# Kernel tuning notes

Measured on AMD Instinct MI355X. Metric: run time of the kernel, lower is better.

## Reference

```python
import jax, jax.numpy as jnp
import numpy as np

N_NODES = 65536
N_EDGES = 262144
N_GRAPHS = 2048
NF = 16   # num_node_features
EF = 6    # num_edge_features
H1, H2, H3 = 32, 16, 8  # conv1 out, conv2 out, lin1 out


def _lin_init(key, fan_in, fan_out):
    kw, kb = jax.random.split(key)
    s = 1.0 / np.sqrt(fan_in)
    w = jax.random.uniform(kw, (fan_in, fan_out), minval=-s, maxval=s, dtype=jnp.float32)
    b = jax.random.uniform(kb, (fan_out,), minval=-s, maxval=s, dtype=jnp.float32)
    return w, b


def setup_inputs() -> dict:
    key = jax.random.key(0)
    ks = jax.random.split(key, 16)
    inp = {}
    inp["x_p"] = jax.random.normal(ks[0], (N_NODES, NF), dtype=jnp.float32)
    inp["x_d"] = jax.random.normal(ks[1], (4, NF), dtype=jnp.float32)  # unused by forward
    inp["edge_attr_p"] = jax.random.uniform(ks[2], (N_EDGES, EF), dtype=jnp.float32)
    inp["edge_attr_d"] = jax.random.uniform(ks[3], (4, EF), dtype=jnp.float32)  # unused
    inp["edge_index_p"] = jax.random.randint(ks[4], (2, N_EDGES), 0, N_NODES, dtype=jnp.int32)
    inp["x_p_batch"] = jnp.sort(jax.random.randint(ks[5], (N_NODES,), 0, N_GRAPHS, dtype=jnp.int32))
    # conv1: NNConv(NF, 32); edge nn: Linear(EF,16) -> ReLU -> Linear(16, NF*32)
    inp["nn1_w1"], inp["nn1_b1"] = _lin_init(ks[6], EF, 16)
    inp["nn1_w2"], inp["nn1_b2"] = _lin_init(ks[7], 16, NF * H1)
    inp["root1"] = _lin_init(ks[8], NF, H1)[0]
    inp["bias1"] = jnp.zeros((H1,), dtype=jnp.float32)
    # conv2: NNConv(32, 16); edge nn: Linear(EF,16) -> ReLU -> Linear(16, 32*16)
    inp["nn2_w1"], inp["nn2_b1"] = _lin_init(ks[9], EF, 16)
    inp["nn2_w2"], inp["nn2_b2"] = _lin_init(ks[10], 16, H1 * H2)
    inp["root2"] = _lin_init(ks[11], H1, H2)[0]
    inp["bias2"] = jnp.zeros((H2,), dtype=jnp.float32)
    # attention pooling gate: Linear(NF,NF) -> ReLU -> Linear(NF,1)
    inp["gate_w1"], inp["gate_b1"] = _lin_init(ks[12], NF, NF)
    inp["gate_w2"], inp["gate_b2"] = _lin_init(ks[13], NF, 1)
    # head: Linear(16+16, 8) -> Linear(8, 1)  (attention=True)
    inp["lin1_w"], inp["lin1_b"] = _lin_init(ks[14], H2 + NF, H3)
    inp["lin2_w"], inp["lin2_b"] = _lin_init(ks[15], H3, 1)
    return inp


def _nnconv(x, edge_attr, src, dst, w1, b1, w2, b2, root, bias, in_c, out_c, n_nodes):
    # per-edge dynamic weight matrix Theta(e) : [E, in_c, out_c]
    h = jax.nn.relu(edge_attr @ w1 + b1) @ w2 + b2
    w_dyn = h.reshape(-1, in_c, out_c)
    msg = jnp.einsum('ei,eio->eo', x[src], w_dyn)          # [E, out_c]
    agg = jax.ops.segment_sum(msg, dst, num_segments=n_nodes)  # scatter-add
    return agg + x @ root + bias


def _attention_pool(x, batch, gw1, gb1, gw2, gb2, n_graphs):
    g = (jax.nn.relu(x @ gw1 + gb1) @ gw2 + gb2)[:, 0]     # [N] gate logits
    m = jax.ops.segment_max(g, batch, num_segments=n_graphs)
    e = jnp.exp(g - m[batch])
    s = jax.ops.segment_sum(e, batch, num_segments=n_graphs)
    alpha = e / s[batch]                                    # per-graph softmax
    return jax.ops.segment_sum(alpha[:, None] * x, batch, num_segments=n_graphs)


def _mean_pool(x, batch, n_graphs):
    s = jax.ops.segment_sum(x, batch, num_segments=n_graphs)
    cnt = jax.ops.segment_sum(jnp.ones((x.shape[0],), x.dtype), batch, num_segments=n_graphs)
    return s / jnp.maximum(cnt, 1.0)[:, None]


def reference(x_p, x_d, edge_attr_p, edge_attr_d, edge_index_p, x_p_batch,
              nn1_w1, nn1_b1, nn1_w2, nn1_b2, root1, bias1,
              nn2_w1, nn2_b1, nn2_w2, nn2_b2, root2, bias2,
              gate_w1, gate_b1, gate_w2, gate_b2,
              lin1_w, lin1_b, lin2_w, lin2_b):
    src, dst = edge_index_p[0], edge_index_p[1]
    # attention pooling on raw node features (attention=True)
    x_att = _attention_pool(x_p, x_p_batch, gate_w1, gate_b1, gate_w2, gate_b2, N_GRAPHS)
    # two NNConv layers with ReLU
    h = jax.nn.relu(_nnconv(x_p, edge_attr_p, src, dst, nn1_w1, nn1_b1, nn1_w2, nn1_b2,
                            root1, bias1, NF, H1, N_NODES))
    h = jax.nn.relu(_nnconv(h, edge_attr_p, src, dst, nn2_w1, nn2_b1, nn2_w2, nn2_b2,
                            root2, bias2, H1, H2, N_NODES))
    g = _mean_pool(h, x_p_batch, N_GRAPHS)                  # [B, 16]
    g = jnp.concatenate([g, x_att], axis=1)                 # [B, 32]
    # dropout p=0.5 is identity in eval mode
    g = g @ lin1_w + lin1_b
    out = g @ lin2_w + lin2_b                               # [B, 1]
    return out
```

## Files before the change

kernel.cpp:

```cpp
#include <hip/hip_runtime.h>

#define NN 65536
#define NE 262144
#define NG 2048

typedef __attribute__((ext_vector_type(16))) float f32x16;
typedef __attribute__((ext_vector_type(4)))  float f32x4;
typedef __attribute__((ext_vector_type(8)))  __bf16 bf16x8;

__device__ inline unsigned pack2(float a, float b) {
    return __builtin_amdgcn_perm(__float_as_uint(b), __float_as_uint(a), 0x07060302u);
}
__device__ inline float lof(float p) {
    return p - __uint_as_float(__float_as_uint(p) & 0xffff0000u);
}
__device__ inline bf16x8 asb(uint4 u) { return __builtin_bit_cast(bf16x8, u); }

__global__ __launch_bounds__(256) void k_setup(
    const int* __restrict__ batch,
    const float* __restrict__ w2a, const float* __restrict__ b2a,
    const float* __restrict__ w2b, const float* __restrict__ b2c,
    int* __restrict__ cnt, int* __restrict__ cur, int* __restrict__ goffs,
    unsigned* __restrict__ f1, unsigned* __restrict__ f2)
{
    int t = blockIdx.x * 256 + threadIdx.x;
    if (t < NN) { cnt[t] = 0; cur[t] = 0; }
    if (t <= NG) {
        int lo = 0, hi = NN;
        while (lo < hi) {
            int mid = (lo + hi) >> 1;
            if (batch[mid] < t) lo = mid + 1; else hi = mid;
        }
        goffs[t] = lo;
    }
    if (t < 17408) {
        int c = t / 8704;
        int r = t - c * 8704;
        int d = r & 3;
        int l = (r >> 2) & 63;
        int tt = (r >> 8) & 1;
        int s = r >> 9;
        if (c == 0) {
            int n = l & 31, g = l >> 5;
            int j0 = 2*d;
            int c0 = (g*8 + j0)*32 + n;
            int c1 = c0 + 32;
            float a = (s < 16) ? w2a[s*512 + c0] : b2a[c0];
            float b = (s < 16) ? w2a[s*512 + c1] : b2a[c1];
            f1[r] = tt ? pack2(lof(a), lof(b)) : pack2(a, b);
        } else {
            int n = l & 15, g = l >> 4;
            int j0 = 2*d;
            int c0 = (g*8 + j0)*16 + n;
            int c1 = c0 + 16;
            float a = (s < 16) ? w2b[s*512 + c0] : b2c[c0];
            float b = (s < 16) ? w2b[s*512 + c1] : b2c[c1];
            f2[r] = tt ? pack2(lof(a), lof(b)) : pack2(a, b);
        }
    }
}

__global__ __launch_bounds__(64) void k_gateatt(const float* __restrict__ x,
    const float* __restrict__ gw1, const float* __restrict__ gb1,
    const float* __restrict__ gw2, const float* __restrict__ gb2,
    const int* __restrict__ goffs, float* __restrict__ x_att)
{
    __shared__ float sw[256];
    __shared__ float sb[16];
    __shared__ float sw2[16];
    __shared__ float sb2;
    __shared__ float gb[1024];
    const int g = blockIdx.x;
    const int lane = threadIdx.x;
    for (int i = lane; i < 256; i += 64) sw[i] = gw1[i];
    if (lane < 16) { sb[lane] = gb1[lane]; sw2[lane] = gw2[lane]; }
    if (lane == 0) sb2 = gb2[0];
    const int s = goffs[g], e = goffs[g + 1];
    const int cnt = e - s;
    if (cnt <= 0) {
        if (lane < 16) x_att[g*16 + lane] = 0.f;
        return;
    }
    const int cap = cnt < 1024 ? cnt : 1024;
    __syncthreads();
    for (int ii = lane; ii < cap; ii += 64) {
        const float4* xp = (const float4*)(x + (size_t)(s + ii) * 16);
        float xv[16];
#pragma unroll
        for (int i = 0; i < 4; ++i) {
            float4 tt = xp[i];
            xv[4*i] = tt.x; xv[4*i+1] = tt.y; xv[4*i+2] = tt.z; xv[4*i+3] = tt.w;
        }
        float gv = sb2;
#pragma unroll
        for (int j = 0; j < 16; ++j) {
            float a = sb[j];
#pragma unroll
            for (int i = 0; i < 16; ++i) a += xv[i] * sw[i*16 + j];
            gv += fmaxf(a, 0.f) * sw2[j];
        }
        gb[ii] = gv;
    }
    __syncthreads();
    float m = -1e30f;
    for (int ii = lane; ii < cap; ii += 64) m = fmaxf(m, gb[ii]);
#pragma unroll
    for (int d = 32; d; d >>= 1) m = fmaxf(m, __shfl_xor(m, d));
    float sum = 0.f;
    for (int ii = lane; ii < cap; ii += 64) {
        float ev = expf(gb[ii] - m);
        gb[ii] = ev;
        sum += ev;
    }
#pragma unroll
    for (int d = 32; d; d >>= 1) sum += __shfl_xor(sum, d);
    const float inv = 1.f / sum;
    __syncthreads();
    const int f = lane & 15, sub = lane >> 4;
    float acc = 0.f;
    for (int ii = sub; ii < cap; ii += 4)
        acc += gb[ii] * inv * x[(size_t)(s + ii)*16 + f];
    acc += __shfl_xor(acc, 16);
    acc += __shfl_xor(acc, 32);
    if (lane < 16) x_att[g*16 + f] = acc;
}

__global__ __launch_bounds__(256) void k_hist(const int* __restrict__ ei, int* __restrict__ cnt)
{
    int e = blockIdx.x * 256 + threadIdx.x;
    if (e >= NE) return;
    atomicAdd(&cnt[ei[NE + e]], 1);
}

__global__ __launch_bounds__(256) void k_scan_blk(const int* __restrict__ cnt,
    int* __restrict__ offs, int* __restrict__ bsum)
{
    __shared__ int s[256];
    int t = threadIdx.x, b = blockIdx.x;
    int v = cnt[b*256 + t];
    s[t] = v;
    __syncthreads();
#pragma unroll
    for (int d = 1; d < 256; d <<= 1) {
        int add = (t >= d) ? s[t - d] : 0;
        __syncthreads();
        s[t] += add;
        __syncthreads();
    }
    offs[b*256 + t] = s[t] - v;
    if (t == 255) bsum[b] = s[255];
}

__global__ __launch_bounds__(256) void k_scan_top(const int* __restrict__ bsum,
    int* __restrict__ boff)
{
    __shared__ int s[256];
    int t = threadIdx.x;
    int v = bsum[t];
    s[t] = v;
    __syncthreads();
#pragma unroll
    for (int d = 1; d < 256; d <<= 1) {
        int add = (t >= d) ? s[t - d] : 0;
        __syncthreads();
        s[t] += add;
        __syncthreads();
    }
    boff[t] = s[t] - v;
}

__global__ __launch_bounds__(256) void k_scan_add(int* __restrict__ offs,
    const int* __restrict__ boff)
{
    int i = blockIdx.x * 256 + threadIdx.x;
    if (i == 0) offs[NN] = NE;
    if (i >= NN) return;
    offs[i] += boff[i >> 8];
}

__global__ __launch_bounds__(256) void k_scatter(const int* __restrict__ ei,
    const int* __restrict__ offs, int* __restrict__ cur,
    int* __restrict__ eperm, int* __restrict__ esrc)
{
    int e = blockIdx.x * 256 + threadIdx.x;
    if (e >= NE) return;
    int d = ei[NE + e];
    int pos = offs[d] + atomicAdd(&cur[d], 1);
    eperm[pos] = e;
    esrc[pos] = ei[e];
}

__global__ __launch_bounds__(256) void k_conv1(
    const float* __restrict__ x, const float* __restrict__ ea,
    const int* __restrict__ eperm, const int* __restrict__ esrc,
    const float* __restrict__ w1, const float* __restrict__ b1,
    const unsigned* __restrict__ bfrag, float* __restrict__ msg)
{
    const int tid  = threadIdx.x;
    const int lane = tid & 63;
    const int wid  = tid >> 6;
    const int m    = lane & 31;
    const int g    = lane >> 5;
    const uint4* bf4 = (const uint4*)bfrag;

    const int tile = blockIdx.x*4 + wid;
    const int p    = tile*32 + m;
    const int src  = esrc[p];
    const int e    = eperm[p];

    float xs[8];
    {
        const float4* xp = (const float4*)(x + (size_t)src*16 + g*8);
        float4 aa = xp[0], bb = xp[1];
        xs[0]=aa.x; xs[1]=aa.y; xs[2]=aa.z; xs[3]=aa.w;
        xs[4]=bb.x; xs[5]=bb.y; xs[6]=bb.z; xs[7]=bb.w;
    }
    float h[17];
    {
        const float2 e01 = *(const float2*)(ea + (size_t)e*6);
        const float2 e23 = *(const float2*)(ea + (size_t)e*6 + 2);
        const float2 e45 = *(const float2*)(ea + (size_t)e*6 + 4);
        const float a0=e01.x, a1=e01.y, a2=e23.x, a3=e23.y, a4=e45.x, a5=e45.y;
#pragma unroll
        for (int j = 0; j < 16; ++j) {
            float c = b1[j];
            c += a0*w1[0*16+j]; c += a1*w1[1*16+j]; c += a2*w1[2*16+j];
            c += a3*w1[3*16+j]; c += a4*w1[4*16+j]; c += a5*w1[5*16+j];
            h[j] = fmaxf(c, 0.f);
        }
        h[16] = 1.f;
    }

    f32x16 acc0 = {}, acc1 = {};
#pragma unroll
    for (int s = 0; s < 17; ++s) {
        const float hs = h[s];
        float p0 = hs*xs[0], p1 = hs*xs[1], p2 = hs*xs[2], p3 = hs*xs[3];
        float p4 = hs*xs[4], p5 = hs*xs[5], p6 = hs*xs[6], p7 = hs*xs[7];
        uint4 uh = { pack2(p0,p1), pack2(p2,p3), pack2(p4,p5), pack2(p6,p7) };
        uint4 ul = { pack2(lof(p0),lof(p1)), pack2(lof(p2),lof(p3)),
                     pack2(lof(p4),lof(p5)), pack2(lof(p6),lof(p7)) };
        uint4 wh = bf4[(s*2+0)*64 + lane];
        uint4 wl = bf4[(s*2+1)*64 + lane];
        if (s & 1) {
            acc1 = __builtin_amdgcn_mfma_f32_32x32x16_bf16(asb(uh), asb(wh), acc1, 0, 0, 0);
            acc1 = __builtin_amdgcn_mfma_f32_32x32x16_bf16(asb(uh), asb(wl), acc1, 0, 0, 0);
            acc1 = __builtin_amdgcn_mfma_f32_32x32x16_bf16(asb(ul), asb(wh), acc1, 0, 0, 0);
        } else {
            acc0 = __builtin_amdgcn_mfma_f32_32x32x16_bf16(asb(uh), asb(wh), acc0, 0, 0, 0);
            acc0 = __builtin_amdgcn_mfma_f32_32x32x16_bf16(asb(uh), asb(wl), acc0, 0, 0, 0);
            acc0 = __builtin_amdgcn_mfma_f32_32x32x16_bf16(asb(ul), asb(wh), acc0, 0, 0, 0);
        }
    }

    float* mbase = msg + (size_t)tile*32*32;
    const int rb = g*4;
#pragma unroll
    for (int r = 0; r < 16; ++r) {
        int mr = (r&3) + 8*(r>>2) + rb;
        mbase[(size_t)mr*32 + m] = acc0[r] + acc1[r];
    }
}

__global__ __launch_bounds__(256) void k_conv2(
    const float* __restrict__ x, const float* __restrict__ ea,
    const int* __restrict__ eperm, const int* __restrict__ esrc,
    const float* __restrict__ w1, const float* __restrict__ b1,
    const unsigned* __restrict__ bfrag, float* __restrict__ msg)
{
    __shared__ float lt[4][16*21];
    const int tid  = threadIdx.x;
    const int lane = tid & 63;
    const int wid  = tid >> 6;
    const int m    = lane & 15;
    const int g    = lane >> 4;
    const uint4* bf4 = (const uint4*)bfrag;

    const int tile = blockIdx.x*4 + wid;
    const int p    = tile*16 + m;
    const int src  = esrc[p];
    const int e    = eperm[p];

    uint4 xh, xl;
    {
        const float4* xp = (const float4*)(x + (size_t)src*32 + g*8);
        float4 aa = xp[0], bb = xp[1];
        float v0=aa.x, v1=aa.y, v2=aa.z, v3=aa.w, v4=bb.x, v5=bb.y, v6=bb.z, v7=bb.w;
        xh = (uint4){ pack2(v0,v1), pack2(v2,v3), pack2(v4,v5), pack2(v6,v7) };
        xl = (uint4){ pack2(lof(v0),lof(v1)), pack2(lof(v2),lof(v3)),
                      pack2(lof(v4),lof(v5)), pack2(lof(v6),lof(v7)) };
    }
    float h[17];
    {
        const float2 e01 = *(const float2*)(ea + (size_t)e*6);
        const float2 e23 = *(const float2*)(ea + (size_t)e*6 + 2);
        const float2 e45 = *(const float2*)(ea + (size_t)e*6 + 4);
        const float a0=e01.x, a1=e01.y, a2=e23.x, a3=e23.y, a4=e45.x, a5=e45.y;
#pragma unroll
        for (int j = 0; j < 16; ++j) {
            float c = b1[j];
            c += a0*w1[0*16+j]; c += a1*w1[1*16+j]; c += a2*w1[2*16+j];
            c += a3*w1[3*16+j]; c += a4*w1[4*16+j]; c += a5*w1[5*16+j];
            h[j] = fmaxf(c, 0.f);
        }
        h[16] = 1.f;
    }

    f32x4 macc = {};
#pragma unroll
    for (int s = 0; s < 17; ++s) {
        uint4 wh = bf4[(s*2+0)*64 + lane];
        uint4 wl = bf4[(s*2+1)*64 + lane];
        f32x4 t = {};
        t = __builtin_amdgcn_mfma_f32_16x16x32_bf16(asb(wh), asb(xh), t, 0, 0, 0);
        t = __builtin_amdgcn_mfma_f32_16x16x32_bf16(asb(wl), asb(xh), t, 0, 0, 0);
        t = __builtin_amdgcn_mfma_f32_16x16x32_bf16(asb(wh), asb(xl), t, 0, 0, 0);
        const float hs = h[s];
        macc.x += hs*t.x; macc.y += hs*t.y; macc.z += hs*t.z; macc.w += hs*t.w;
    }

    float* lw = lt[wid];
    lw[m*21 + g*4 + 0] = macc.x;
    lw[m*21 + g*4 + 1] = macc.y;
    lw[m*21 + g*4 + 2] = macc.z;
    lw[m*21 + g*4 + 3] = macc.w;
    asm volatile("s_waitcnt lgkmcnt(0)" ::: "memory");
    const int rrow = lane >> 2, fq = lane & 3;
    float o0 = lw[rrow*21 + fq*4 + 0];
    float o1 = lw[rrow*21 + fq*4 + 1];
    float o2 = lw[rrow*21 + fq*4 + 2];
    float o3 = lw[rrow*21 + fq*4 + 3];
    float4* mb = (float4*)(msg + (size_t)tile*256);
    mb[rrow*4 + fq] = make_float4(o0, o1, o2, o3);
}

__global__ __launch_bounds__(256) void k_reduce1(
    const float* __restrict__ msg, const int* __restrict__ offs,
    const float* __restrict__ x, const float* __restrict__ root,
    const float* __restrict__ bias, float* __restrict__ h1)
{
    __shared__ float s_r[512];
    __shared__ float s_b[32];
    int tid = threadIdx.x;
    for (int i = tid; i < 512; i += 256) s_r[i] = root[i];
    if (tid < 32) s_b[tid] = bias[tid];
    __syncthreads();
    int gid = blockIdx.x * 256 + tid;
    int n = gid >> 3, q = gid & 7;
    int s = offs[n], e = offs[n + 1];
    float4 acc = make_float4(s_b[4*q], s_b[4*q+1], s_b[4*q+2], s_b[4*q+3]);
    const float4* s_r4 = (const float4*)s_r;
    const float* xp = x + (size_t)n * 16;
#pragma unroll
    for (int i = 0; i < 16; ++i) {
        float xi = xp[i];
        float4 w = s_r4[i*8 + q];
        acc.x += xi*w.x; acc.y += xi*w.y; acc.z += xi*w.z; acc.w += xi*w.w;
    }
    for (int p = s; p < e; ++p) {
        float4 mr = ((const float4*)(msg + (size_t)p * 32))[q];
        acc.x += mr.x; acc.y += mr.y; acc.z += mr.z; acc.w += mr.w;
    }
    acc.x = fmaxf(acc.x, 0.f); acc.y = fmaxf(acc.y, 0.f);
    acc.z = fmaxf(acc.z, 0.f); acc.w = fmaxf(acc.w, 0.f);
    ((float4*)(h1 + (size_t)n * 32))[q] = acc;
}

__global__ __launch_bounds__(256) void k_reduce2(
    const float* __restrict__ msg, const int* __restrict__ offs,
    const float* __restrict__ h1, const float* __restrict__ root,
    const float* __restrict__ bias, float* __restrict__ h2)
{
    __shared__ float s_r[512];
    __shared__ float s_b[16];
    int tid = threadIdx.x;
    for (int i = tid; i < 512; i += 256) s_r[i] = root[i];
    if (tid < 16) s_b[tid] = bias[tid];
    __syncthreads();
    int gid = blockIdx.x * 256 + tid;
    int n = gid >> 2, q = gid & 3;
    int s = offs[n], e = offs[n + 1];
    float4 acc = make_float4(s_b[4*q], s_b[4*q+1], s_b[4*q+2], s_b[4*q+3]);
    const float4* s_r4 = (const float4*)s_r;
    const float* xp = h1 + (size_t)n * 32;
#pragma unroll
    for (int i = 0; i < 32; ++i) {
        float xi = xp[i];
        float4 w = s_r4[i*4 + q];
        acc.x += xi*w.x; acc.y += xi*w.y; acc.z += xi*w.z; acc.w += xi*w.w;
    }
    for (int p = s; p < e; ++p) {
        float4 mr = ((const float4*)(msg + (size_t)p * 16))[q];
        acc.x += mr.x; acc.y += mr.y; acc.z += mr.z; acc.w += mr.w;
    }
    acc.x = fmaxf(acc.x, 0.f); acc.y = fmaxf(acc.y, 0.f);
    acc.z = fmaxf(acc.z, 0.f); acc.w = fmaxf(acc.w, 0.f);
    ((float4*)(h2 + (size_t)n * 16))[q] = acc;
}

__global__ __launch_bounds__(64) void k_head(
    const float* __restrict__ h2, const float* __restrict__ x_att,
    const int* __restrict__ goffs,
    const float* __restrict__ l1w, const float* __restrict__ l1b,
    const float* __restrict__ l2w, const float* __restrict__ l2b,
    float* __restrict__ out)
{
    int g = blockIdx.x;
    int lane = threadIdx.x;
    int s = goffs[g], e = goffs[g + 1];
    __shared__ float v[32];
    __shared__ float hmid[8];
    int f = lane & 15, sub = lane >> 4;
    float acc = 0.f;
    for (int i = s + sub; i < e; i += 4) acc += h2[(size_t)i*16 + f];
    acc += __shfl_xor(acc, 16);
    acc += __shfl_xor(acc, 32);
    float cnt = fmaxf((float)(e - s), 1.0f);
    if (lane < 16) {
        v[lane]      = acc / cnt;
        v[16 + lane] = x_att[g*16 + lane];
    }
    __syncthreads();
    if (lane < 8) {
        float a = l1b[lane];
#pragma unroll
        for (int i = 0; i < 32; ++i) a += v[i] * l1w[i*8 + lane];
        hmid[lane] = a;
    }
    __syncthreads();
    if (lane == 0) {
        float a = l2b[0];
#pragma unroll
        for (int j = 0; j < 8; ++j) a += hmid[j] * l2w[j];
        out[g] = a;
    }
}

extern "C" void kernel_launch(void* const* d_in, const int* in_sizes, int n_in,
                              void* d_out, int out_size, void* d_ws, size_t ws_size,
                              hipStream_t stream) {
    const float* x_p    = (const float*)d_in[0];
    const float* ea_p   = (const float*)d_in[2];
    const int*   ei     = (const int*)d_in[4];
    const int*   batch  = (const int*)d_in[5];
    const float* nn1_w1 = (const float*)d_in[6];
    const float* nn1_b1 = (const float*)d_in[7];
    const float* nn1_w2 = (const float*)d_in[8];
    const float* nn1_b2 = (const float*)d_in[9];
    const float* root1  = (const float*)d_in[10];
    const float* bias1  = (const float*)d_in[11];
    const float* nn2_w1 = (const float*)d_in[12];
    const float* nn2_b1 = (const float*)d_in[13];
    const float* nn2_w2 = (const float*)d_in[14];
    const float* nn2_b2 = (const float*)d_in[15];
    const float* root2  = (const float*)d_in[16];
    const float* bias2  = (const float*)d_in[17];
    const float* gw1    = (const float*)d_in[18];
    const float* gb1    = (const float*)d_in[19];
    const float* gw2    = (const float*)d_in[20];
    const float* gb2    = (const float*)d_in[21];
    const float* l1w    = (const float*)d_in[22];
    const float* l1b    = (const float*)d_in[23];
    const float* l2w    = (const float*)d_in[24];
    const float* l2b    = (const float*)d_in[25];

    float*    h1     = (float*)d_ws;
    float*    h2     = h1 + (size_t)NN * 32;
    float*    x_att  = h2 + (size_t)NN * 16;
    int*      goffs  = (int*)(x_att + (size_t)NG * 16);
    int*      offs   = goffs + 2052;
    int*      cnt    = offs + 65540;
    int*      cur    = cnt + NN;
    int*      bsum   = cur + NN;
    int*      boff   = bsum + 256;
    int*      eperm  = boff + 256;
    int*      esrc   = eperm + NE;
    unsigned* bfrag1 = (unsigned*)(esrc + NE);
    unsigned* bfrag2 = bfrag1 + 8704;
    float*    msg    = (float*)(bfrag2 + 8704);

    k_setup<<<512, 256, 0, stream>>>(batch, nn1_w2, nn1_b2, nn2_w2, nn2_b2,
                                     cnt, cur, goffs, bfrag1, bfrag2);

    k_gateatt<<<NG, 64, 0, stream>>>(x_p, gw1, gb1, gw2, gb2, goffs, x_att);

    k_hist<<<NE/256, 256, 0, stream>>>(ei, cnt);
    k_scan_blk<<<NN/256, 256, 0, stream>>>(cnt, offs, bsum);
    k_scan_top<<<1, 256, 0, stream>>>(bsum, boff);
    k_scan_add<<<NN/256, 256, 0, stream>>>(offs, boff);
    k_scatter<<<NE/256, 256, 0, stream>>>(ei, offs, cur, eperm, esrc);

    k_conv1<<<2048, 256, 0, stream>>>(x_p, ea_p, eperm, esrc, nn1_w1, nn1_b1, bfrag1, msg);
    k_reduce1<<<NN*8/256, 256, 0, stream>>>(msg, offs, x_p, root1, bias1, h1);

    k_conv2<<<4096, 256, 0, stream>>>(h1, ea_p, eperm, esrc, nn2_w1, nn2_b1, bfrag2, msg);
    k_reduce2<<<NN*4/256, 256, 0, stream>>>(msg, offs, h1, root2, bias2, h2);

    k_head<<<NG, 64, 0, stream>>>(h2, x_att, goffs, l1w, l1b, l2w, l2b, (float*)d_out);
}
```

Measured before the change: 138.3 us.

## Factor edge weight out of conv1 MFMA, pack edge pairs, stage msg via LDS

In conv1 the per-edge hidden scalar is now applied after the matrix multiply. The MFMA computes W_s·x once per hidden slot and the result is scaled by h[s] in registers, so the per-step product, bf16 packing and hi/lo split are gone and x is converted only once. Edge permutation and source index are merged into one int2 array, so each conv kernel reads one coalesced word. Conv1 output is transposed through shared memory so messages are written with float4 stores, and both conv kernels get an occupancy hint in their launch bounds. This costs 16 extra vector FMAs per step and extra LDS traffic, and the change in operand roles and precision-split order could shift numerics slightly.

Result: slower. 391.7 us (+183.3%).

```diff
diff --git a/kernel.cpp b/kernel.cpp
--- a/kernel.cpp
+++ b/kernel.cpp
@@ -179,23 +179,22 @@
 }
 
 __global__ __launch_bounds__(256) void k_scatter(const int* __restrict__ ei,
-    const int* __restrict__ offs, int* __restrict__ cur,
-    int* __restrict__ eperm, int* __restrict__ esrc)
+    const int* __restrict__ offs, int* __restrict__ cur, int2* __restrict__ epair)
 {
     int e = blockIdx.x * 256 + threadIdx.x;
     if (e >= NE) return;
     int d = ei[NE + e];
     int pos = offs[d] + atomicAdd(&cur[d], 1);
-    eperm[pos] = e;
-    esrc[pos] = ei[e];
-}
-
-__global__ __launch_bounds__(256) void k_conv1(
+    epair[pos] = make_int2(e, ei[e]);
+}
+
+__global__ __launch_bounds__(256, 4) void k_conv1(
     const float* __restrict__ x, const float* __restrict__ ea,
-    const int* __restrict__ eperm, const int* __restrict__ esrc,
+    const int2* __restrict__ epair,
     const float* __restrict__ w1, const float* __restrict__ b1,
     const unsigned* __restrict__ bfrag, float* __restrict__ msg)
 {
+    __shared__ float lt[4][32*33];
     const int tid  = threadIdx.x;
     const int lane = tid & 63;
     const int wid  = tid >> 6;
@@ -205,15 +204,16 @@
 
     const int tile = blockIdx.x*4 + wid;
     const int p    = tile*32 + m;
-    const int src  = esrc[p];
-    const int e    = eperm[p];
-
-    float xs[8];
+    const int2 ep  = epair[p];
+    const int e    = ep.x, src = ep.y;
+
+    uint4 xh, xl;
     {
         const float4* xp = (const float4*)(x + (size_t)src*16 + g*8);
         float4 aa = xp[0], bb = xp[1];
-        xs[0]=aa.x; xs[1]=aa.y; xs[2]=aa.z; xs[3]=aa.w;
-        xs[4]=bb.x; xs[5]=bb.y; xs[6]=bb.z; xs[7]=bb.w;
+        xh = (uint4){ pack2(aa.x,aa.y), pack2(aa.z,aa.w), pack2(bb.x,bb.y), pack2(bb.z,bb.w) };
+        xl = (uint4){ pack2(lof(aa.x),lof(aa.y)), pack2(lof(aa.z),lof(aa.w)),
+                      pack2(lof(bb.x),lof(bb.y)), pack2(lof(bb.z),lof(bb.w)) };
     }
     float h[17];
     {
@@ -231,40 +231,40 @@
         h[16] = 1.f;
     }
 
-    f32x16 acc0 = {}, acc1 = {};
+    f32x16 acc = {};
 #pragma unroll
     for (int s = 0; s < 17; ++s) {
-        const float hs = h[s];
-        float p0 = hs*xs[0], p1 = hs*xs[1], p2 = hs*xs[2], p3 = hs*xs[3];
-        float p4 = hs*xs[4], p5 = hs*xs[5], p6 = hs*xs[6], p7 = hs*xs[7];
-        uint4 uh = { pack2(p0,p1), pack2(p2,p3), pack2(p4,p5), pack2(p6,p7) };
-        uint4 ul = { pack2(lof(p0),lof(p1)), pack2(lof(p2),lof(p3)),
-                     pack2(lof(p4),lof(p5)), pack2(lof(p6),lof(p7)) };
         uint4 wh = bf4[(s*2+0)*64 + lane];
         uint4 wl = bf4[(s*2+1)*64 + lane];
-        if (s & 1) {
-            acc1 = __builtin_amdgcn_mfma_f32_32x32x16_bf16(asb(uh), asb(wh), acc1, 0, 0, 0);
-            acc1 = __builtin_amdgcn_mfma_f32_32x32x16_bf16(asb(uh), asb(wl), acc1, 0, 0, 0);
-            acc1 = __builtin_amdgcn_mfma_f32_32x32x16_bf16(asb(ul), asb(wh), acc1, 0, 0, 0);
-        } else {
-            acc0 = __builtin_amdgcn_mfma_f32_32x32x16_bf16(asb(uh), asb(wh), acc0, 0, 0, 0);
-            acc0 = __builtin_amdgcn_mfma_f32_32x32x16_bf16(asb(uh), asb(wl), acc0, 0, 0, 0);
-            acc0 = __builtin_amdgcn_mfma_f32_32x32x16_bf16(asb(ul), asb(wh), acc0, 0, 0, 0);
-        }
-    }
-
-    float* mbase = msg + (size_t)tile*32*32;
-    const int rb = g*4;
+        f32x16 t = {};
+        t = __builtin_amdgcn_mfma_f32_32x32x16_bf16(asb(wh), asb(xh), t, 0, 0, 0);
+        t = __builtin_amdgcn_mfma_f32_32x32x16_bf16(asb(wl), asb(xh), t, 0, 0, 0);
+        t = __builtin_amdgcn_mfma_f32_32x32x16_bf16(asb(wh), asb(xl), t, 0, 0, 0);
+        const float hs = h[s];
+#pragma unroll
+        for (int r = 0; r < 16; ++r) acc[r] += hs * t[r];
+    }
+
+    float* lw = lt[wid];
 #pragma unroll
     for (int r = 0; r < 16; ++r) {
-        int mr = (r&3) + 8*(r>>2) + rb;
-        mbase[(size_t)mr*32 + m] = acc0[r] + acc1[r];
-    }
-}
-
-__global__ __launch_bounds__(256) void k_conv2(
+        int o = (r&3) + 8*(r>>2) + 4*g;
+        lw[m*33 + o] = acc[r];
+    }
+    asm volatile("s_waitcnt lgkmcnt(0)" ::: "memory");
+    const int er = lane >> 1, hf = lane & 1;
+    float vv[16];
+#pragma unroll
+    for (int k = 0; k < 16; ++k) vv[k] = lw[er*33 + hf*16 + k];
+    float4* mb = (float4*)(msg + (size_t)tile*1024 + er*32 + hf*16);
+#pragma unroll
+    for (int j = 0; j < 4; ++j)
+        mb[j] = make_float4(vv[4*j], vv[4*j+1], vv[4*j+2], vv[4*j+3]);
+}
+
+__global__ __launch_bounds__(256, 4) void k_conv2(
     const float* __restrict__ x, const float* __restrict__ ea,
-    const int* __restrict__ eperm, const int* __restrict__ esrc,
+    const int2* __restrict__ epair,
     const float* __restrict__ w1, const float* __restrict__ b1,
     const unsigned* __restrict__ bfrag, float* __restrict__ msg)
 {
@@ -278,17 +278,16 @@
 
     const int tile = blockIdx.x*4 + wid;
     const int p    = tile*16 + m;
-    const int src  = esrc[p];
-    const int e    = eperm[p];
+    const int2 ep  = epair[p];
+    const int e    = ep.x, src = ep.y;
 
     uint4 xh, xl;
     {
         const float4* xp = (const float4*)(x + (size_t)src*32 + g*8);
         float4 aa = xp[0], bb = xp[1];
-        float v0=aa.x, v1=aa.y, v2=aa.z, v3=aa.w, v4=bb.x, v5=bb.y, v6=bb.z, v7=bb.w;
-        xh = (uint4){ pack2(v0,v1), pack2(v2,v3), pack2(v4,v5), pack2(v6,v7) };
-        xl = (uint4){ pack2(lof(v0),lof(v1)), pack2(lof(v2),lof(v3)),
-                      pack2(lof(v4),lof(v5)), pack2(lof(v6),lof(v7)) };
+        xh = (uint4){ pack2(aa.x,aa.y), pack2(aa.z,aa.w), pack2(bb.x,bb.y), pack2(bb.z,bb.w) };
+        xl = (uint4){ pack2(lof(aa.x),lof(aa.y)), pack2(lof(aa.z),lof(aa.w)),
+                      pack2(lof(bb.x),lof(bb.y)), pack2(lof(bb.z),lof(bb.w)) };
     }
     float h[17];
     {
@@ -473,9 +472,8 @@
     int*      cur    = cnt + NN;
     int*      bsum   = cur + NN;
     int*      boff   = bsum + 256;
-    int*      eperm  = boff + 256;
-    int*      esrc   = eperm + NE;
-    unsigned* bfrag1 = (unsigned*)(esrc + NE);
+    int2*     epair  = (int2*)(boff + 256);
+    unsigned* bfrag1 = (unsigned*)(epair + NE);
     unsigned* bfrag2 = bfrag1 + 8704;
     float*    msg    = (float*)(bfrag2 + 8704);
 
@@ -488,12 +486,12 @@
     k_scan_blk<<<NN/256, 256, 0, stream>>>(cnt, offs, bsum);
     k_scan_top<<<1, 256, 0, stream>>>(bsum, boff);
     k_scan_add<<<NN/256, 256, 0, stream>>>(offs, boff);
-    k_scatter<<<NE/256, 256, 0, stream>>>(ei, offs, cur, eperm, esrc);
-
-    k_conv1<<<2048, 256, 0, stream>>>(x_p, ea_p, eperm, esrc, nn1_w1, nn1_b1, bfrag1, msg);
+    k_scatter<<<NE/256, 256, 0, stream>>>(ei, offs, cur, epair);
+
+    k_conv1<<<2048, 256, 0, stream>>>(x_p, ea_p, epair, nn1_w1, nn1_b1, bfrag1, msg);
     k_reduce1<<<NN*8/256, 256, 0, stream>>>(msg, offs, x_p, root1, bias1, h1);
 
-    k_conv2<<<4096, 256, 0, stream>>>(h1, ea_p, eperm, esrc, nn2_w1, nn2_b1, bfrag2, msg);
+    k_conv2<<<4096, 256, 0, stream>>>(h1, ea_p, epair, nn2_w1, nn2_b1, bfrag2, msg);
     k_reduce2<<<NN*4/256, 256, 0, stream>>>(msg, offs, h1, root2, bias2, h2);
 
     k_head<<<NG, 64, 0, stream>>>(h2, x_att, goffs, l1w, l1b, l2w, l2b, (float*)d_out);
```
